# Kernel tuning notes

Hardware: AMD Instinct MI355X
Metric: run time of the kernel (lower is better)

Reference implementation:

```python
import jax, jax.numpy as jnp
import numpy as np


def _lin_weights(n_out, n_ctrl):
    # Sparse bilinear interpolation matrix [n_out, n_ctrl]: control points are
    # spread over [0, n_out-1] at positions linspace(0, n_ctrl-1, n_out) in grid coords.
    u = jnp.linspace(0.0, n_ctrl - 1.0, n_out)
    i0 = jnp.clip(jnp.floor(u), 0, n_ctrl - 2).astype(jnp.int32)
    f = u - i0.astype(u.dtype)
    W = jnp.zeros((n_out, n_ctrl), dtype=jnp.float32)
    rows = jnp.arange(n_out)
    W = W.at[rows, i0].set(1.0 - f)
    W = W.at[rows, i0 + 1].add(f)
    return W


def setup_inputs() -> dict:
    key = jax.random.key(0)
    k1, k2 = jax.random.split(key)
    inputs = jax.random.uniform(k1, (2048, 4096, 3), dtype=jnp.float32)
    displacement = jax.random.normal(k2, (2, 3, 3), dtype=jnp.float32)
    return {"inputs": inputs, "displacement": displacement}


def reference(inputs, displacement):
    H, W, C = inputs.shape
    disp = displacement * 5.0  # matches tf.random.normal([2,3,3]) * 5
    Wy = _lin_weights(H, disp.shape[1])  # [H, 3]
    Wx = _lin_weights(W, disp.shape[2])  # [W, 3]
    # Upsample 3x3 control grid to dense per-pixel displacement field [2, H, W]
    dense = jnp.einsum('hy,dyx,wx->dhw', Wy, disp, Wx)
    cy = jnp.arange(H, dtype=inputs.dtype)[:, None] + dense[0]  # [H, W]
    cx = jnp.arange(W, dtype=inputs.dtype)[None, :] + dense[1]  # [H, W]
    cval = jax.lax.stop_gradient(jnp.max(inputs))  # tf.get_static_value(max)

    y0 = jnp.floor(cy)
    x0 = jnp.floor(cx)
    fy = (cy - y0)[..., None]  # [H, W, 1]
    fx = (cx - x0)[..., None]
    y0i = y0.astype(jnp.int32)
    x0i = x0.astype(jnp.int32)

    def corner(yi, xi):
        # order=1 sampling, mode='constant': out-of-bounds samples -> cval
        valid = (yi >= 0) & (yi < H) & (xi >= 0) & (xi < W)
        yc = jnp.clip(yi, 0, H - 1)
        xc = jnp.clip(xi, 0, W - 1)
        v = inputs[yc, xc]  # gather -> [H, W, C]
        return jnp.where(valid[..., None], v, cval)

    v00 = corner(y0i, x0i)
    v01 = corner(y0i, x0i + 1)
    v10 = corner(y0i + 1, x0i)
    v11 = corner(y0i + 1, x0i + 1)

    out = (v00 * (1.0 - fy) * (1.0 - fx)
           + v01 * (1.0 - fy) * fx
           + v10 * fy * (1.0 - fx)
           + v11 * fy * fx)
    return out
```

## Files before the change

### kernel.cpp

```cpp
#include <hip/hip_runtime.h>

#define H_DIM 2048
#define W_DIM 4096
#define N_ELEM (H_DIM * W_DIM * 3)
#define N_PIX  (H_DIM * W_DIM)

__global__ __launch_bounds__(256) void max_reduce_kernel(const float* __restrict__ in,
                                                         unsigned int* __restrict__ ws) {
    const float4* __restrict__ in4 = (const float4*)in;
    int t = blockIdx.x * 256 + threadIdx.x;
    float m = 0.0f;
    #pragma unroll
    for (int j = 0; j < 6; j++) {
        float4 v[8];
        #pragma unroll
        for (int k = 0; k < 8; k++)
            v[k] = in4[t + (j * 8 + k) * 131072];
        #pragma unroll
        for (int k = 0; k < 8; k++)
            m = fmaxf(m, fmaxf(fmaxf(v[k].x, v[k].y), fmaxf(v[k].z, v[k].w)));
    }
    #pragma unroll
    for (int off = 32; off > 0; off >>= 1)
        m = fmaxf(m, __shfl_down(m, off, 64));
    __shared__ float smax[4];
    int lane = threadIdx.x & 63;
    int wave = threadIdx.x >> 6;
    if (lane == 0) smax[wave] = m;
    __syncthreads();
    if (threadIdx.x == 0) {
        float bm = fmaxf(fmaxf(smax[0], smax[1]), fmaxf(smax[2], smax[3]));
        atomicMax(ws, __float_as_uint(bm));
    }
}

struct F3 { float a, b, c; };

__global__ __launch_bounds__(256) void elastic_sample_kernel(const float* __restrict__ in,
                                                             const float* __restrict__ disp,
                                                             const unsigned int* __restrict__ wsmax,
                                                             float* __restrict__ out) {
    __shared__ __align__(16) float obuf[768];
    int tid = threadIdx.x;
    int t = blockIdx.x * 256 + tid;
    int y = t >> 12;
    int x = t & (W_DIM - 1);

    float cval = __uint_as_float(*wsmax);

    float uy = (float)y * (2.0f / (float)(H_DIM - 1));
    float ux = (float)x * (2.0f / (float)(W_DIM - 1));
    int iy = min((int)uy, 1);
    int ix = min((int)ux, 1);
    float fyc = uy - (float)iy;
    float fxc = ux - (float)ix;

    const float* dp0 = disp + iy * 3 + ix;
    const float* dp1 = dp0 + 9;
    float dy = 5.0f * ((1.0f - fyc) * ((1.0f - fxc) * dp0[0] + fxc * dp0[1])
                     +         fyc  * ((1.0f - fxc) * dp0[3] + fxc * dp0[4]));
    float dx = 5.0f * ((1.0f - fyc) * ((1.0f - fxc) * dp1[0] + fxc * dp1[1])
                     +         fyc  * ((1.0f - fxc) * dp1[3] + fxc * dp1[4]));

    float cy = (float)y + dy;
    float cx = (float)x + dx;
    float y0f = floorf(cy);
    float x0f = floorf(cx);
    float fy = cy - y0f;
    float fx = cx - x0f;
    int y0 = (int)y0f;
    int x0 = (int)x0f;

    int xbase = min(max(x0, 0), W_DIM - 2);
    bool sel = (x0 == xbase);
    bool vx0 = (x0 >= 0) & (x0 <= W_DIM - 1);
    bool vx1 = (x0 >= -1) & (x0 <= W_DIM - 2);

    float acc0 = 0.0f, acc1 = 0.0f, acc2 = 0.0f;
    #pragma unroll
    for (int j = 0; j < 2; j++) {
        int yy = y0 + j;
        bool vy = (yy >= 0) & (yy < H_DIM);
        int yr = min(max(yy, 0), H_DIM - 1);
        const float* p = in + ((size_t)yr * W_DIM + xbase) * 3;
        F3 L0 = *(const F3*)p;
        F3 L1 = *(const F3*)(p + 3);

        float wj = j ? fy : (1.0f - fy);
        float w0 = wj * (1.0f - fx);
        float w1 = wj * fx;
        bool v0 = vy & vx0;
        bool v1 = vy & vx1;

        float c0a = sel ? L0.a : L1.a;  float c1a = sel ? L1.a : L0.a;
        float c0b = sel ? L0.b : L1.b;  float c1b = sel ? L1.b : L0.b;
        float c0c = sel ? L0.c : L1.c;  float c1c = sel ? L1.c : L0.c;
        c0a = v0 ? c0a : cval;  c1a = v1 ? c1a : cval;
        c0b = v0 ? c0b : cval;  c1b = v1 ? c1b : cval;
        c0c = v0 ? c0c : cval;  c1c = v1 ? c1c : cval;

        acc0 = fmaf(w0, c0a, fmaf(w1, c1a, acc0));
        acc1 = fmaf(w0, c0b, fmaf(w1, c1b, acc1));
        acc2 = fmaf(w0, c0c, fmaf(w1, c1c, acc2));
    }

    obuf[tid * 3 + 0] = acc0;
    obuf[tid * 3 + 1] = acc1;
    obuf[tid * 3 + 2] = acc2;
    __syncthreads();
    if (tid < 192) {
        float4 v = ((const float4*)obuf)[tid];
        ((float4*)out)[(size_t)blockIdx.x * 192 + tid] = v;
    }
}

extern "C" void kernel_launch(void* const* d_in, const int* in_sizes, int n_in,
                              void* d_out, int out_size, void* d_ws, size_t ws_size,
                              hipStream_t stream) {
    const float* in   = (const float*)d_in[0];
    const float* disp = (const float*)d_in[1];
    float* out = (float*)d_out;
    unsigned int* wsmax = (unsigned int*)d_ws;

    hipMemsetAsync(d_ws, 0, sizeof(unsigned int), stream);

    max_reduce_kernel<<<512, 256, 0, stream>>>(in, wsmax);

    elastic_sample_kernel<<<N_PIX / 256, 256, 0, stream>>>(in, disp, wsmax, out);
}
```

Baseline: 64.87 us.

## Stage per-block source window in shared memory with coalesced float4 loads

```diff
diff --git a/kernel.cpp b/kernel.cpp
--- a/kernel.cpp
+++ b/kernel.cpp
@@ -2,8 +2,12 @@
 
 #define H_DIM 2048
 #define W_DIM 4096
-#define N_ELEM (H_DIM * W_DIM * 3)
-#define N_PIX  (H_DIM * W_DIM)
+#define ROWF  (W_DIM * 3)
+#define ROW4  (ROWF / 4)
+#define NROW_CAP 8
+#define NPX_CAP  272
+#define NF_CAP   (NPX_CAP * 3)
+#define NF4_CAP  (NF_CAP / 4)
 
 __global__ __launch_bounds__(256) void max_reduce_kernel(const float* __restrict__ in,
                                                          unsigned int* __restrict__ ws) {
@@ -14,8 +18,7 @@
     for (int j = 0; j < 6; j++) {
         float4 v[8];
         #pragma unroll
-        for (int k = 0; k < 8; k++)
-            v[k] = in4[t + (j * 8 + k) * 131072];
+        for (int k = 0; k < 8; k++) v[k] = in4[t + (j * 8 + k) * 131072];
         #pragma unroll
         for (int k = 0; k < 8; k++)
             m = fmaxf(m, fmaxf(fmaxf(v[k].x, v[k].y), fmaxf(v[k].z, v[k].w)));
@@ -24,44 +27,62 @@
     for (int off = 32; off > 0; off >>= 1)
         m = fmaxf(m, __shfl_down(m, off, 64));
     __shared__ float smax[4];
-    int lane = threadIdx.x & 63;
-    int wave = threadIdx.x >> 6;
-    if (lane == 0) smax[wave] = m;
+    if ((threadIdx.x & 63) == 0) smax[threadIdx.x >> 6] = m;
     __syncthreads();
-    if (threadIdx.x == 0) {
-        float bm = fmaxf(fmaxf(smax[0], smax[1]), fmaxf(smax[2], smax[3]));
-        atomicMax(ws, __float_as_uint(bm));
-    }
+    if (threadIdx.x == 0)
+        atomicMax(ws, __float_as_uint(fmaxf(fmaxf(smax[0], smax[1]), fmaxf(smax[2], smax[3]))));
 }
 
-struct F3 { float a, b, c; };
+__device__ __forceinline__ void eval_disp(const float* __restrict__ disp,
+                                          int iy, float fyc, int xx,
+                                          float& dy, float& dx) {
+    float ux = (float)xx * (2.0f / 4095.0f);
+    int ix = min((int)ux, 1);
+    float fxc = ux - (float)ix;
+    const float* dp0 = disp + iy * 3 + ix;
+    const float* dp1 = dp0 + 9;
+    dy = 5.0f * ((1.0f - fyc) * ((1.0f - fxc) * dp0[0] + fxc * dp0[1])
+               +          fyc  * ((1.0f - fxc) * dp0[3] + fxc * dp0[4]));
+    dx = 5.0f * ((1.0f - fyc) * ((1.0f - fxc) * dp1[0] + fxc * dp1[1])
+               +          fyc  * ((1.0f - fxc) * dp1[3] + fxc * dp1[4]));
+}
 
 __global__ __launch_bounds__(256) void elastic_sample_kernel(const float* __restrict__ in,
                                                              const float* __restrict__ disp,
                                                              const unsigned int* __restrict__ wsmax,
                                                              float* __restrict__ out) {
-    __shared__ __align__(16) float obuf[768];
-    int tid = threadIdx.x;
-    int t = blockIdx.x * 256 + tid;
-    int y = t >> 12;
-    int x = t & (W_DIM - 1);
+    __shared__ __align__(16) float stage[NROW_CAP * NF_CAP];
+    const int tid = threadIdx.x;
+    const int bid = blockIdx.x;
+    const int y  = bid >> 4;
+    const int xs = (bid & 15) << 8;
+    const int x  = xs + tid;
 
-    float cval = __uint_as_float(*wsmax);
+    const float cval = __uint_as_float(*wsmax);
 
-    float uy = (float)y * (2.0f / (float)(H_DIM - 1));
-    float ux = (float)x * (2.0f / (float)(W_DIM - 1));
+    float uy = (float)y * (2.0f / 2047.0f);
     int iy = min((int)uy, 1);
-    int ix = min((int)ux, 1);
     float fyc = uy - (float)iy;
-    float fxc = ux - (float)ix;
 
-    const float* dp0 = disp + iy * 3 + ix;
-    const float* dp1 = dp0 + 9;
-    float dy = 5.0f * ((1.0f - fyc) * ((1.0f - fxc) * dp0[0] + fxc * dp0[1])
-                     +         fyc  * ((1.0f - fxc) * dp0[3] + fxc * dp0[4]));
-    float dx = 5.0f * ((1.0f - fyc) * ((1.0f - fxc) * dp1[0] + fxc * dp1[1])
-                     +         fyc  * ((1.0f - fxc) * dp1[3] + fxc * dp1[4]));
+    float dyA, dxA, dyB, dxB;
+    eval_disp(disp, iy, fyc, xs,        dyA, dxA);
+    eval_disp(disp, iy, fyc, xs + 255,  dyB, dxB);
+    float sY = (dyB - dyA) * (1.0f / 255.0f);
+    float sX = (dxB - dxA) * (1.0f / 255.0f);
 
+    float cyMin = (float)y + fminf(dyA, dyB);
+    float cyMax = (float)y + fmaxf(dyA, dyB);
+    float cxMin = (float)xs + dxA;
+    float cxMax = (float)(xs + 255) + dxB;
+
+    int ymin_s = (int)floorf(cyMin);
+    int nrows  = (int)floorf(cyMax) - ymin_s + 2;
+    int xmin_s = ((int)floorf(cxMin)) & ~3;
+    int npx    = (int)floorf(cxMax) + 2 - xmin_s;
+    bool fits  = (nrows <= NROW_CAP) && (npx <= NPX_CAP);
+
+    float dy = fmaf((float)tid, sY, dyA);
+    float dx = fmaf((float)tid, sX, dxA);
     float cy = (float)y + dy;
     float cx = (float)x + dx;
     float y0f = floorf(cy);
@@ -71,47 +92,76 @@
     int y0 = (int)y0f;
     int x0 = (int)x0f;
 
-    int xbase = min(max(x0, 0), W_DIM - 2);
-    bool sel = (x0 == xbase);
-    bool vx0 = (x0 >= 0) & (x0 <= W_DIM - 1);
-    bool vx1 = (x0 >= -1) & (x0 <= W_DIM - 2);
+    float s00a, s00b, s00c, s01a, s01b, s01c;
+    float s10a, s10b, s10c, s11a, s11b, s11c;
 
-    float acc0 = 0.0f, acc1 = 0.0f, acc2 = 0.0f;
-    #pragma unroll
-    for (int j = 0; j < 2; j++) {
-        int yy = y0 + j;
-        bool vy = (yy >= 0) & (yy < H_DIM);
-        int yr = min(max(yy, 0), H_DIM - 1);
-        const float* p = in + ((size_t)yr * W_DIM + xbase) * 3;
-        F3 L0 = *(const F3*)p;
-        F3 L1 = *(const F3*)(p + 3);
+    if (fits) {
+        int nf4 = (npx * 3 + 3) >> 2;
+        int gb4 = (xmin_s * 3) / 4;
+        bool tload = tid < nf4;
+        int c4 = gb4 + tid;
+        bool cOOB = (c4 < 0) | (c4 >= ROW4);
+        int c4c = min(max(c4, 0), ROW4 - 1);
 
-        float wj = j ? fy : (1.0f - fy);
-        float w0 = wj * (1.0f - fx);
-        float w1 = wj * fx;
-        bool v0 = vy & vx0;
-        bool v1 = vy & vx1;
+        float4 tv[NROW_CAP];
+        #pragma unroll
+        for (int r = 0; r < NROW_CAP; r++) {
+            if (r < nrows && tload) {
+                int yc = min(max(ymin_s + r, 0), H_DIM - 1);
+                tv[r] = ((const float4*)in)[(size_t)yc * ROW4 + c4c];
+            }
+        }
+        #pragma unroll
+        for (int r = 0; r < NROW_CAP; r++) {
+            if (r < nrows && tload) {
+                bool rOOB = ((ymin_s + r) < 0) | ((ymin_s + r) >= H_DIM);
+                bool oob = rOOB | cOOB;
+                float4 v = tv[r];
+                if (oob) { v.x = cval; v.y = cval; v.z = cval; v.w = cval; }
+                ((float4*)stage)[r * NF4_CAP + tid] = v;
+            }
+        }
+        __syncthreads();
 
-        float c0a = sel ? L0.a : L1.a;  float c1a = sel ? L1.a : L0.a;
-        float c0b = sel ? L0.b : L1.b;  float c1b = sel ? L1.b : L0.b;
-        float c0c = sel ? L0.c : L1.c;  float c1c = sel ? L1.c : L0.c;
-        c0a = v0 ? c0a : cval;  c1a = v1 ? c1a : cval;
-        c0b = v0 ? c0b : cval;  c1b = v1 ? c1b : cval;
-        c0c = v0 ? c0c : cval;  c1c = v1 ? c1c : cval;
-
-        acc0 = fmaf(w0, c0a, fmaf(w1, c1a, acc0));
-        acc1 = fmaf(w0, c0b, fmaf(w1, c1b, acc1));
-        acc2 = fmaf(w0, c0c, fmaf(w1, c1c, acc2));
+        int r0 = min(max(y0 - ymin_s, 0), nrows - 2);
+        int j0 = min(max(x0 - xmin_s, 0), npx - 2);
+        const float* p0 = stage + r0 * NF_CAP + j0 * 3;
+        const float* p1 = p0 + NF_CAP;
+        s00a = p0[0]; s00b = p0[1]; s00c = p0[2];
+        s01a = p0[3]; s01b = p0[4]; s01c = p0[5];
+        s10a = p1[0]; s10b = p1[1]; s10c = p1[2];
+        s11a = p1[3]; s11b = p1[4]; s11c = p1[5];
+    } else {
+        bool vy0 = (y0 >= 0) & (y0 < H_DIM);
+        bool vy1 = (y0 >= -1) & (y0 < H_DIM - 1);
+        bool vx0 = (x0 >= 0) & (x0 < W_DIM);
+        bool vx1 = (x0 >= -1) & (x0 < W_DIM - 1);
+        int yc0 = min(max(y0, 0), H_DIM - 1);
+        int yc1 = min(max(y0 + 1, 0), H_DIM - 1);
+        int xc0 = min(max(x0, 0), W_DIM - 1);
+        int xc1 = min(max(x0 + 1, 0), W_DIM - 1);
+        const float* q00 = in + ((size_t)yc0 * W_DIM + xc0) * 3;
+        const float* q01 = in + ((size_t)yc0 * W_DIM + xc1) * 3;
+        const float* q10 = in + ((size_t)yc1 * W_DIM + xc0) * 3;
+        const float* q11 = in + ((size_t)yc1 * W_DIM + xc1) * 3;
+        bool v00 = vy0 & vx0, v01 = vy0 & vx1, v10 = vy1 & vx0, v11 = vy1 & vx1;
+        s00a = v00 ? q00[0] : cval; s00b = v00 ? q00[1] : cval; s00c = v00 ? q00[2] : cval;
+        s01a = v01 ? q01[0] : cval; s01b = v01 ? q01[1] : cval; s01c = v01 ? q01[2] : cval;
+        s10a = v10 ? q10[0] : cval; s10b = v10 ? q10[1] : cval; s10c = v10 ? q10[2] : cval;
+        s11a = v11 ? q11[0] : cval; s11b = v11 ? q11[1] : cval; s11c = v11 ? q11[2] : cval;
     }
 
-    obuf[tid * 3 + 0] = acc0;
-    obuf[tid * 3 + 1] = acc1;
-    obuf[tid * 3 + 2] = acc2;
-    __syncthreads();
-    if (tid < 192) {
-        float4 v = ((const float4*)obuf)[tid];
-        ((float4*)out)[(size_t)blockIdx.x * 192 + tid] = v;
-    }
+    float g0 = 1.0f - fy, h0 = 1.0f - fx;
+    float w00 = g0 * h0, w01 = g0 * fx, w10 = fy * h0, w11 = fy * fx;
+
+    float acc0 = fmaf(w00, s00a, fmaf(w01, s01a, fmaf(w10, s10a, w11 * s11a)));
+    float acc1 = fmaf(w00, s00b, fmaf(w01, s01b, fmaf(w10, s10b, w11 * s11b)));
+    float acc2 = fmaf(w00, s00c, fmaf(w01, s01c, fmaf(w10, s10c, w11 * s11c)));
+
+    float* o = out + ((size_t)y * W_DIM + x) * 3;
+    o[0] = acc0;
+    o[1] = acc1;
+    o[2] = acc2;
 }
 
 extern "C" void kernel_launch(void* const* d_in, const int* in_sizes, int n_in,
@@ -126,5 +176,5 @@
 
     max_reduce_kernel<<<512, 256, 0, stream>>>(in, wsmax);
 
-    elastic_sample_kernel<<<N_PIX / 256, 256, 0, stream>>>(in, disp, wsmax, out);
+    elastic_sample_kernel<<<32768, 256, 0, stream>>>(in, disp, wsmax, out);
 }
```

Measured after the change: 64.45 us. About the same (-0.6%).

## Replace atomic max with two-stage reduction, remap sample blocks across XCD bands, nontemporal stores

Applied to the files above, without the earlier changes.

```diff
diff --git a/kernel.cpp b/kernel.cpp
--- a/kernel.cpp
+++ b/kernel.cpp
@@ -2,20 +2,22 @@
 
 #define H_DIM 2048
 #define W_DIM 4096
-#define N_ELEM (H_DIM * W_DIM * 3)
-#define N_PIX  (H_DIM * W_DIM)
 
-__global__ __launch_bounds__(256) void max_reduce_kernel(const float* __restrict__ in,
-                                                         unsigned int* __restrict__ ws) {
+typedef float fx4 __attribute__((ext_vector_type(4)));
+
+#define WS_PART_OFF 64
+#define MAXP_BLOCKS 1024
+
+__global__ __launch_bounds__(256) void max_partial_kernel(const float* __restrict__ in,
+                                                          float* __restrict__ wsf) {
     const float4* __restrict__ in4 = (const float4*)in;
     int t = blockIdx.x * 256 + threadIdx.x;
     float m = 0.0f;
     #pragma unroll
-    for (int j = 0; j < 6; j++) {
+    for (int j = 0; j < 3; j++) {
         float4 v[8];
         #pragma unroll
-        for (int k = 0; k < 8; k++)
-            v[k] = in4[t + (j * 8 + k) * 131072];
+        for (int k = 0; k < 8; k++) v[k] = in4[t + (j * 8 + k) * (MAXP_BLOCKS * 256)];
         #pragma unroll
         for (int k = 0; k < 8; k++)
             m = fmaxf(m, fmaxf(fmaxf(v[k].x, v[k].y), fmaxf(v[k].z, v[k].w)));
@@ -24,37 +26,49 @@
     for (int off = 32; off > 0; off >>= 1)
         m = fmaxf(m, __shfl_down(m, off, 64));
     __shared__ float smax[4];
-    int lane = threadIdx.x & 63;
-    int wave = threadIdx.x >> 6;
-    if (lane == 0) smax[wave] = m;
+    if ((threadIdx.x & 63) == 0) smax[threadIdx.x >> 6] = m;
     __syncthreads();
-    if (threadIdx.x == 0) {
-        float bm = fmaxf(fmaxf(smax[0], smax[1]), fmaxf(smax[2], smax[3]));
-        atomicMax(ws, __float_as_uint(bm));
-    }
+    if (threadIdx.x == 0)
+        wsf[WS_PART_OFF + blockIdx.x] = fmaxf(fmaxf(smax[0], smax[1]), fmaxf(smax[2], smax[3]));
+}
+
+__global__ __launch_bounds__(256) void max_final_kernel(float* __restrict__ wsf) {
+    const float4* p4 = (const float4*)(wsf + WS_PART_OFF);
+    float4 v = p4[threadIdx.x];
+    float m = fmaxf(fmaxf(v.x, v.y), fmaxf(v.z, v.w));
+    #pragma unroll
+    for (int off = 32; off > 0; off >>= 1)
+        m = fmaxf(m, __shfl_down(m, off, 64));
+    __shared__ float smax[4];
+    if ((threadIdx.x & 63) == 0) smax[threadIdx.x >> 6] = m;
+    __syncthreads();
+    if (threadIdx.x == 0)
+        wsf[0] = fmaxf(fmaxf(smax[0], smax[1]), fmaxf(smax[2], smax[3]));
 }
 
 struct F3 { float a, b, c; };
 
 __global__ __launch_bounds__(256) void elastic_sample_kernel(const float* __restrict__ in,
                                                              const float* __restrict__ disp,
-                                                             const unsigned int* __restrict__ wsmax,
+                                                             const float* __restrict__ wsf,
                                                              float* __restrict__ out) {
     __shared__ __align__(16) float obuf[768];
-    int tid = threadIdx.x;
-    int t = blockIdx.x * 256 + tid;
-    int y = t >> 12;
-    int x = t & (W_DIM - 1);
+    const int tid = threadIdx.x;
+    int bid = blockIdx.x;
+    int band = bid & 7;
+    int idx = bid >> 3;
+    int y  = (band << 8) + (idx >> 4);
+    int xs = (idx & 15) << 8;
+    int x  = xs + tid;
 
-    float cval = __uint_as_float(*wsmax);
+    const float cval = wsf[0];
 
-    float uy = (float)y * (2.0f / (float)(H_DIM - 1));
-    float ux = (float)x * (2.0f / (float)(W_DIM - 1));
+    float uy = (float)y * (2.0f / 2047.0f);
+    float ux = (float)x * (2.0f / 4095.0f);
     int iy = min((int)uy, 1);
     int ix = min((int)ux, 1);
     float fyc = uy - (float)iy;
     float fxc = ux - (float)ix;
-
     const float* dp0 = disp + iy * 3 + ix;
     const float* dp1 = dp0 + 9;
     float dy = 5.0f * ((1.0f - fyc) * ((1.0f - fxc) * dp0[0] + fxc * dp0[1])
@@ -109,8 +123,9 @@
     obuf[tid * 3 + 2] = acc2;
     __syncthreads();
     if (tid < 192) {
-        float4 v = ((const float4*)obuf)[tid];
-        ((float4*)out)[(size_t)blockIdx.x * 192 + tid] = v;
+        fx4 v = ((const fx4*)obuf)[tid];
+        fx4* dst = ((fx4*)out) + ((size_t)y * W_DIM + xs) * 3 / 4 + tid;
+        __builtin_nontemporal_store(v, dst);
     }
 }
 
@@ -120,11 +135,9 @@
     const float* in   = (const float*)d_in[0];
     const float* disp = (const float*)d_in[1];
     float* out = (float*)d_out;
-    unsigned int* wsmax = (unsigned int*)d_ws;
+    float* wsf = (float*)d_ws;
 
-    hipMemsetAsync(d_ws, 0, sizeof(unsigned int), stream);
-
-    max_reduce_kernel<<<512, 256, 0, stream>>>(in, wsmax);
-
-    elastic_sample_kernel<<<N_PIX / 256, 256, 0, stream>>>(in, disp, wsmax, out);
+    max_partial_kernel<<<MAXP_BLOCKS, 256, 0, stream>>>(in, wsf);
+    max_final_kernel<<<1, 256, 0, stream>>>(wsf);
+    elastic_sample_kernel<<<32768, 256, 0, stream>>>(in, disp, wsf, out);
 }
```

After: 62.46 us. -3.7%, faster.
